# Kernel optimization log

Hardware: AMD Instinct MI355X
Metric: run time of the kernel (lower is better)

The kernel has to match this reference:

```python
import jax, jax.numpy as jnp
import numpy as np

# Custom floating-point formats (mptorch qpt.float_quantize, nearest, subnormals, no saturate)
EXP_W, MAN_W = 4, 3      # weight_quant / input_quant (e4m3)
EXP_MAC, MAN_MAC = 5, 10 # fwd MAC / bias format (e5m10, fp16-like)

B, S, D = 8, 2048, 1024
H = 4 * D


def float_quantize(x, exp, man):
    """Round x to nearest value in a float format with `exp` exponent bits and
    `man` mantissa bits, with subnormals, no saturation (overflow -> inf)."""
    bias = 2 ** (exp - 1) - 1
    min_exp = 1 - bias                      # smallest normal exponent
    max_val = (2.0 - 2.0 ** (-man)) * 2.0 ** bias
    ax = jnp.abs(x)
    e = jnp.floor(jnp.log2(jnp.where(ax > 0, ax, 1.0)))
    e = jnp.maximum(e, float(min_exp))      # clamp -> subnormal spacing
    scale = jnp.exp2(e - man)               # ulp at this exponent
    q = jnp.round(x / scale) * scale        # round-half-to-even, like 'nearest'
    q = jnp.where(jnp.abs(q) > max_val, jnp.sign(x) * jnp.inf, q)
    return jnp.where(ax == 0, x, q)


def setup_inputs() -> dict:
    key = jax.random.key(0)
    k = jax.random.split(key, 5)
    return {
        "x": jax.random.normal(k[0], (B, S, D), dtype=jnp.float32),
        "w1": jax.random.normal(k[1], (H, D), dtype=jnp.float32) * 0.02,
        "b1": jax.random.normal(k[2], (H,), dtype=jnp.float32) * 0.02,
        "w2": jax.random.normal(k[3], (D, H), dtype=jnp.float32) * 0.02,
        "b2": jax.random.normal(k[4], (D,), dtype=jnp.float32) * 0.02,
    }


def reference(x, w1, b1, w2, b2):
    # nn.Linear + ReLU (full precision)
    h = jax.nn.relu(jnp.einsum('bsd,hd->bsh', x, w1) + b1)
    # QLinear: quantize input and weight to e4m3, bias to MAC format,
    # accumulate, then quantize the result to the fwd MAC format.
    hq = float_quantize(h, EXP_W, MAN_W)
    wq = float_quantize(w2, EXP_W, MAN_W)
    bq = float_quantize(b2, EXP_MAC, MAN_MAC)
    out = jnp.einsum('bsh,dh->bsd', hq, wq) + bq
    out = float_quantize(out, EXP_MAC, MAN_MAC)
    # Dropout(0.2) is identity at inference.
    return out
```

## Files before the change

### kernel.cpp

```cpp
#include <hip/hip_runtime.h>
#include <stdint.h>


#define M_TOT 16384
#define D_DIM 1024
#define H_DIM 4096

typedef _Float16 f16x8 __attribute__((ext_vector_type(8)));
typedef _Float16 f16x4 __attribute__((ext_vector_type(4)));
typedef float f32x4 __attribute__((ext_vector_type(4)));
typedef int i32x4 __attribute__((ext_vector_type(4)));
typedef int i32x8 __attribute__((ext_vector_type(8)));

__device__ __forceinline__ void gl16(const void* g, void* l) {
    __builtin_amdgcn_global_load_lds(
        (const __attribute__((address_space(1))) unsigned int*)(uintptr_t)g,
        (__attribute__((address_space(3))) unsigned int*)(unsigned int)(uintptr_t)l,
        16, 0, 0);
}

__device__ __forceinline__ _Float16 q_e4m3_pos(float v) {
    uint32_t t = __float_as_uint(v);
    uint32_t tn = (t + 0x7ffffu + ((t >> 20) & 1u)) & 0xfff00000u;
    float qn = __uint_as_float(tn);
    float qs = rintf(v * 512.0f) * 0.001953125f;
    return (_Float16)(v < 0.015625f ? qs : qn);
}

__global__ __launch_bounds__(256) void cvt_f16_kernel(
    const float* __restrict__ in, _Float16* __restrict__ out, int n4)
{
    int i = blockIdx.x * 256 + threadIdx.x;
    if (i >= n4) return;
    float4 v = reinterpret_cast<const float4*>(in)[i];
    f16x4 hv = {(_Float16)v.x, (_Float16)v.y, (_Float16)v.z, (_Float16)v.w};
    reinterpret_cast<f16x4*>(out)[i] = hv;
}

__global__ __launch_bounds__(256) void quant_e4m3_byte_kernel(
    const float* __restrict__ in, uint32_t* __restrict__ outq, int n4)
{
    int i = blockIdx.x * 256 + threadIdx.x;
    if (i >= n4) return;
    float4 v = reinterpret_cast<const float4*>(in)[i];
    uint32_t r = __builtin_amdgcn_cvt_pk_fp8_f32(v.x, v.y, 0, false);
    r = __builtin_amdgcn_cvt_pk_fp8_f32(v.z, v.w, r, true);
    outq[i] = r;
}

__global__ __launch_bounds__(512) void gemm1_f16(
    const _Float16* __restrict__ A, const _Float16* __restrict__ B,
    const float* __restrict__ bias, uint8_t* __restrict__ Cq)
{
    constexpr int K = D_DIM;
    constexpr int N = H_DIM;
    __shared__ __align__(16) _Float16 smem[65536];
    _Float16* sA = smem;
    _Float16* sB = smem + 32768;

    const int tid  = threadIdx.x;
    const int lane = tid & 63;
    const int w    = tid >> 6;
    const int wr   = w >> 2, wc = w & 3;
    const int fr   = lane & 15, kq = lane >> 4;

    constexpr int NBX = N / 256;
    constexpr int NWG = (M_TOT / 256) * NBX;
    constexpr int CPX = NWG / 8;
    int bid = blockIdx.y * NBX + blockIdx.x;
    bid = (bid & 7) * CPX + (bid >> 3);
    const int n0 = (bid % NBX) * 256;
    const int m0 = (bid / NBX) * 256;

    const int srow = tid >> 3;
    const int sseg = (tid & 7) ^ (srow & 7);
    const _Float16* gA = A + (size_t)(m0 + srow) * K + sseg * 8;
    const _Float16* gB = B + (size_t)(n0 + srow) * K + sseg * 8;
    const int ldsw = w * 512;
    const size_t R1 = (size_t)64 * K, R2 = (size_t)128 * K, R3 = (size_t)192 * K;

    const int xorv = fr & 7;
    const int cA0 = (kq ^ xorv) * 8;
    const int cA1 = ((kq + 4) ^ xorv) * 8;
    const int aRow = wr * 128 + fr;
    const int bRow = wc * 64 + fr;

    f32x4 acc[8][4];
#pragma unroll
    for (int i = 0; i < 8; i++)
#pragma unroll
        for (int j = 0; j < 4; j++) acc[i][j] = (f32x4){0.f, 0.f, 0.f, 0.f};

    f16x8 bfr[4][2];
    constexpr int NK = K / 64;

    gl16(gB,      sB + ldsw);
    gl16(gB + R1, sB + 4096 + ldsw);
    gl16(gB + R2, sB + 8192 + ldsw);
    gl16(gB + R3, sB + 12288 + ldsw);
    gl16(gA,      sA + ldsw);
    gl16(gA + R1, sA + 4096 + ldsw);
    gl16(gA + R2, sA + 8192 + ldsw);
    gl16(gA + R3, sA + 12288 + ldsw);
    asm volatile("s_waitcnt vmcnt(0)" ::: "memory");
    __builtin_amdgcn_s_barrier();
    asm volatile("" ::: "memory");

    for (int t = 0; t < NK; ++t) {
        const int c = t & 1;
        const _Float16* sAc = sA + c * 16384;
        const _Float16* sBc = sB + c * 16384;
        _Float16* sAn = sA + (c ^ 1) * 16384;
        _Float16* sBn = sB + (c ^ 1) * 16384;
        const bool pref = (t + 1 < NK);

        if (pref) {
            const _Float16* gAn = gA + (size_t)(t + 1) * 64;
            const _Float16* gBn = gB + (size_t)(t + 1) * 64;
            gl16(gBn,      sBn + ldsw);
            gl16(gBn + R1, sBn + 4096 + ldsw);
            gl16(gBn + R2, sBn + 8192 + ldsw);
            gl16(gBn + R3, sBn + 12288 + ldsw);
            gl16(gAn,      sAn + ldsw);
            gl16(gAn + R1, sAn + 4096 + ldsw);
            gl16(gAn + R2, sAn + 8192 + ldsw);
            gl16(gAn + R3, sAn + 12288 + ldsw);
        }

#pragma unroll
        for (int p = 0; p < 4; ++p) {
            f16x8 afr[2][2];
#pragma unroll
            for (int ii = 0; ii < 2; ii++) {
                const _Float16* ra = sAc + (aRow + (2 * p + ii) * 16) * 64;
                afr[ii][0] = *(const f16x8*)(ra + cA0);
                afr[ii][1] = *(const f16x8*)(ra + cA1);
            }
            if (p == 0) {
#pragma unroll
                for (int j = 0; j < 4; j++) {
                    const _Float16* rb = sBc + (bRow + j * 16) * 64;
                    bfr[j][0] = *(const f16x8*)(rb + cA0);
                    bfr[j][1] = *(const f16x8*)(rb + cA1);
                }
            }
            __builtin_amdgcn_s_setprio(1);
#pragma unroll
            for (int ii = 0; ii < 2; ii++)
#pragma unroll
                for (int j = 0; j < 4; j++) {
                    acc[2*p+ii][j] = __builtin_amdgcn_mfma_f32_16x16x32_f16(
                        afr[ii][0], bfr[j][0], acc[2*p+ii][j], 0, 0, 0);
                    acc[2*p+ii][j] = __builtin_amdgcn_mfma_f32_16x16x32_f16(
                        afr[ii][1], bfr[j][1], acc[2*p+ii][j], 0, 0, 0);
                }
            __builtin_amdgcn_s_setprio(0);
        }

        asm volatile("s_waitcnt vmcnt(0)" ::: "memory");
        __builtin_amdgcn_s_barrier();
        asm volatile("" ::: "memory");
    }

    const int col0 = n0 + wc * 64 + fr;
    float bv[4];
#pragma unroll
    for (int j = 0; j < 4; j++) bv[j] = bias[col0 + j * 16];
    const int sub = (fr & 7) * 2;
    const int slotbase = wc * 8 + (fr >> 3);
    const int rowbase = wr * 128 + kq * 4;
#pragma unroll
    for (int i = 0; i < 8; i++) {
        const int trow0 = rowbase + i * 16;
#pragma unroll
        for (int r = 0; r < 4; r++) {
            const int trow = trow0 + r;
            const int swz = (((kq & 1) * 4 + r)) ^ (kq >> 1);
#pragma unroll
            for (int j = 0; j < 4; j++) {
                float v = fmaxf(acc[i][j][r] + bv[j], 0.0f);
                _Float16 q = q_e4m3_pos(v);
                int byte = trow * 512 + (((slotbase + j * 2) ^ swz) << 4) + sub;
                *(_Float16*)((char*)smem + byte) = q;
            }
        }
    }
    __syncthreads();
#pragma unroll
    for (int cch = 0; cch < 16; cch++) {
        int flat = cch * 512 + tid;
        int row  = flat >> 5;
        int slot = flat & 31;
        int swz  = (row & 7) ^ ((row >> 3) & 1);
        f16x8 v8 = *(const f16x8*)((char*)smem + row * 512 + ((slot ^ swz) << 4));
        uint32_t u0 = __builtin_amdgcn_cvt_pk_fp8_f32((float)v8[0], (float)v8[1], 0, false);
        u0 = __builtin_amdgcn_cvt_pk_fp8_f32((float)v8[2], (float)v8[3], u0, true);
        uint32_t u1 = __builtin_amdgcn_cvt_pk_fp8_f32((float)v8[4], (float)v8[5], 0, false);
        u1 = __builtin_amdgcn_cvt_pk_fp8_f32((float)v8[6], (float)v8[7], u1, true);
        uint2 u = {u0, u1};
        *(uint2*)(Cq + (size_t)(m0 + row) * N + n0 + slot * 8) = u;
    }
}

__global__ __launch_bounds__(512) void gemm2_fp8(
    const uint8_t* __restrict__ A, const uint8_t* __restrict__ B,
    const float* __restrict__ b2, float* __restrict__ C)
{
    constexpr int Kb = H_DIM;
    constexpr int N  = D_DIM;
    __shared__ __align__(16) uint8_t smem[131072];
    uint8_t* sA = smem;
    uint8_t* sB = smem + 65536;

    const int tid  = threadIdx.x;
    const int lane = tid & 63;
    const int w    = tid >> 6;
    const int wr   = w >> 2, wc = w & 3;
    const int fr   = lane & 15, kq = lane >> 4;

    constexpr int NBX = N / 256;
    constexpr int NWG = (M_TOT / 256) * NBX;
    constexpr int CPX = NWG / 8;
    int bid = blockIdx.y * NBX + blockIdx.x;
    bid = (bid & 7) * CPX + (bid >> 3);
    const int n0 = (bid % NBX) * 256;
    const int m0 = (bid / NBX) * 256;

    const int srow = tid >> 3;
    const int sseg = (tid & 7) ^ (srow & 7);
    const uint8_t* gA = A + (size_t)(m0 + srow) * Kb + sseg * 16;
    const uint8_t* gB = B + (size_t)(n0 + srow) * Kb + sseg * 16;
    const int ldsw = w * 1024;
    const size_t R1 = (size_t)64 * Kb, R2 = (size_t)128 * Kb, R3 = (size_t)192 * Kb;

    const int xorv = fr & 7;
    const int sO0 = ((2 * kq) ^ xorv) * 16;
    const int sO1 = ((2 * kq + 1) ^ xorv) * 16;
    const int aRowB = (wr * 128 + fr) * 128;
    const int bRowB = (wc * 64 + fr) * 128;

    f32x4 acc[8][4];
#pragma unroll
    for (int i = 0; i < 8; i++)
#pragma unroll
        for (int j = 0; j < 4; j++) acc[i][j] = (f32x4){0.f, 0.f, 0.f, 0.f};

    i32x8 bfr[4];
    constexpr int NK = Kb / 128;
    constexpr uint32_t SC1 = 0x7f7f7f7fu;

    gl16(gB,      sB + ldsw);
    gl16(gB + R1, sB + 8192 + ldsw);
    gl16(gB + R2, sB + 16384 + ldsw);
    gl16(gB + R3, sB + 24576 + ldsw);
    gl16(gA,      sA + ldsw);
    gl16(gA + R1, sA + 8192 + ldsw);
    gl16(gA + R2, sA + 16384 + ldsw);
    gl16(gA + R3, sA + 24576 + ldsw);
    asm volatile("s_waitcnt vmcnt(0)" ::: "memory");
    __builtin_amdgcn_s_barrier();
    asm volatile("" ::: "memory");

    for (int t = 0; t < NK; ++t) {
        const int c = t & 1;
        const uint8_t* sAc = sA + c * 32768;
        const uint8_t* sBc = sB + c * 32768;
        uint8_t* sAn = sA + (c ^ 1) * 32768;
        uint8_t* sBn = sB + (c ^ 1) * 32768;
        const bool pref = (t + 1 < NK);

        if (pref) {
            const uint8_t* gAn = gA + (size_t)(t + 1) * 128;
            const uint8_t* gBn = gB + (size_t)(t + 1) * 128;
            gl16(gBn,      sBn + ldsw);
            gl16(gBn + R1, sBn + 8192 + ldsw);
            gl16(gBn + R2, sBn + 16384 + ldsw);
            gl16(gBn + R3, sBn + 24576 + ldsw);
            gl16(gAn,      sAn + ldsw);
            gl16(gAn + R1, sAn + 8192 + ldsw);
            gl16(gAn + R2, sAn + 16384 + ldsw);
            gl16(gAn + R3, sAn + 24576 + ldsw);
        }

#pragma unroll
        for (int p = 0; p < 4; ++p) {
            i32x8 af[2];
#pragma unroll
            for (int ii = 0; ii < 2; ii++) {
                const uint8_t* ra = sAc + aRowB + (2 * p + ii) * 2048;
                i32x4 lo = *(const i32x4*)(ra + sO0);
                i32x4 hi = *(const i32x4*)(ra + sO1);
                af[ii] = (i32x8){lo.x, lo.y, lo.z, lo.w, hi.x, hi.y, hi.z, hi.w};
            }
            if (p == 0) {
#pragma unroll
                for (int j = 0; j < 4; j++) {
                    const uint8_t* rb = sBc + bRowB + j * 2048;
                    i32x4 lo = *(const i32x4*)(rb + sO0);
                    i32x4 hi = *(const i32x4*)(rb + sO1);
                    bfr[j] = (i32x8){lo.x, lo.y, lo.z, lo.w, hi.x, hi.y, hi.z, hi.w};
                }
            }
            __builtin_amdgcn_s_setprio(1);
#pragma unroll
            for (int ii = 0; ii < 2; ii++)
#pragma unroll
                for (int j = 0; j < 4; j++) {
                    acc[2*p+ii][j] = __builtin_amdgcn_mfma_scale_f32_16x16x128_f8f6f4(
                        af[ii], bfr[j], acc[2*p+ii][j],
                        0, 0,
                        0, SC1,
                        0, SC1);
                }
            __builtin_amdgcn_s_setprio(0);
        }

        asm volatile("s_waitcnt vmcnt(0)" ::: "memory");
        __builtin_amdgcn_s_barrier();
        asm volatile("" ::: "memory");
    }

    const int col0 = n0 + wc * 64 + fr;
    const int row0 = m0 + wr * 128 + kq * 4;
#pragma unroll
    for (int j = 0; j < 4; j++) {
        const float bq = (float)(_Float16)b2[col0 + j * 16];
#pragma unroll
        for (int i = 0; i < 8; i++) {
            size_t base = (size_t)(row0 + i * 16) * N + (col0 + j * 16);
#pragma unroll
            for (int r = 0; r < 4; r++) {
                float v = acc[i][j][r] + bq;
                C[base + (size_t)r * N] = (float)(_Float16)v;
            }
        }
    }
}

extern "C" void kernel_launch(void* const* d_in, const int* in_sizes, int n_in,
                              void* d_out, int out_size, void* d_ws, size_t ws_size,
                              hipStream_t stream) {
    const float* x  = (const float*)d_in[0];
    const float* w1 = (const float*)d_in[1];
    const float* b1 = (const float*)d_in[2];
    const float* w2 = (const float*)d_in[3];
    const float* b2 = (const float*)d_in[4];
    float* out = (float*)d_out;

    const size_t need = 67108864ull + 33554432ull + 8388608ull + 4194304ull;
    if (ws_size < need) return;

    char* ws = (char*)d_ws;
    uint8_t*  hq  = (uint8_t*)ws;
    _Float16* xh  = (_Float16*)(ws + 67108864ull);
    _Float16* w1h = xh + 16777216;
    uint8_t*  wq  = (uint8_t*)(w1h + 4194304);

    cvt_f16_kernel<<<16384, 256, 0, stream>>>(x, xh, 4194304);
    cvt_f16_kernel<<<4096, 256, 0, stream>>>(w1, w1h, 1048576);
    quant_e4m3_byte_kernel<<<4096, 256, 0, stream>>>(w2, (uint32_t*)wq, 1048576);

    gemm1_f16<<<dim3(H_DIM / 256, M_TOT / 256), 512, 0, stream>>>(xh, w1h, b1, hq);
    gemm2_fp8<<<dim3(D_DIM / 256, M_TOT / 256), 512, 0, stream>>>(hq, wq, b2, out);
}
```

Before: 246.2 us.

## Single-buffer gemm1 LDS and split epilogue staging to halve shared memory

```diff
diff --git a/kernel.cpp b/kernel.cpp
--- a/kernel.cpp
+++ b/kernel.cpp
@@ -48,15 +48,15 @@
     outq[i] = r;
 }
 
-__global__ __launch_bounds__(512) void gemm1_f16(
+__global__ __launch_bounds__(512, 4) void gemm1_f16(
     const _Float16* __restrict__ A, const _Float16* __restrict__ B,
     const float* __restrict__ bias, uint8_t* __restrict__ Cq)
 {
     constexpr int K = D_DIM;
     constexpr int N = H_DIM;
-    __shared__ __align__(16) _Float16 smem[65536];
+    __shared__ __align__(16) _Float16 smem[32768];
     _Float16* sA = smem;
-    _Float16* sB = smem + 32768;
+    _Float16* sB = smem + 16384;
 
     const int tid  = threadIdx.x;
     const int lane = tid & 63;
@@ -107,39 +107,19 @@
     asm volatile("" ::: "memory");
 
     for (int t = 0; t < NK; ++t) {
-        const int c = t & 1;
-        const _Float16* sAc = sA + c * 16384;
-        const _Float16* sBc = sB + c * 16384;
-        _Float16* sAn = sA + (c ^ 1) * 16384;
-        _Float16* sBn = sB + (c ^ 1) * 16384;
-        const bool pref = (t + 1 < NK);
-
-        if (pref) {
-            const _Float16* gAn = gA + (size_t)(t + 1) * 64;
-            const _Float16* gBn = gB + (size_t)(t + 1) * 64;
-            gl16(gBn,      sBn + ldsw);
-            gl16(gBn + R1, sBn + 4096 + ldsw);
-            gl16(gBn + R2, sBn + 8192 + ldsw);
-            gl16(gBn + R3, sBn + 12288 + ldsw);
-            gl16(gAn,      sAn + ldsw);
-            gl16(gAn + R1, sAn + 4096 + ldsw);
-            gl16(gAn + R2, sAn + 8192 + ldsw);
-            gl16(gAn + R3, sAn + 12288 + ldsw);
-        }
-
 #pragma unroll
         for (int p = 0; p < 4; ++p) {
             f16x8 afr[2][2];
 #pragma unroll
             for (int ii = 0; ii < 2; ii++) {
-                const _Float16* ra = sAc + (aRow + (2 * p + ii) * 16) * 64;
+                const _Float16* ra = sA + (aRow + (2 * p + ii) * 16) * 64;
                 afr[ii][0] = *(const f16x8*)(ra + cA0);
                 afr[ii][1] = *(const f16x8*)(ra + cA1);
             }
             if (p == 0) {
 #pragma unroll
                 for (int j = 0; j < 4; j++) {
-                    const _Float16* rb = sBc + (bRow + j * 16) * 64;
+                    const _Float16* rb = sB + (bRow + j * 16) * 64;
                     bfr[j][0] = *(const f16x8*)(rb + cA0);
                     bfr[j][1] = *(const f16x8*)(rb + cA1);
                 }
@@ -157,9 +137,25 @@
             __builtin_amdgcn_s_setprio(0);
         }
 
-        asm volatile("s_waitcnt vmcnt(0)" ::: "memory");
+        asm volatile("" ::: "memory");
         __builtin_amdgcn_s_barrier();
         asm volatile("" ::: "memory");
+
+        if (t + 1 < NK) {
+            const _Float16* gAn = gA + (size_t)(t + 1) * 64;
+            const _Float16* gBn = gB + (size_t)(t + 1) * 64;
+            gl16(gBn,      sB + ldsw);
+            gl16(gBn + R1, sB + 4096 + ldsw);
+            gl16(gBn + R2, sB + 8192 + ldsw);
+            gl16(gBn + R3, sB + 12288 + ldsw);
+            gl16(gAn,      sA + ldsw);
+            gl16(gAn + R1, sA + 4096 + ldsw);
+            gl16(gAn + R2, sA + 8192 + ldsw);
+            gl16(gAn + R3, sA + 12288 + ldsw);
+            asm volatile("s_waitcnt vmcnt(0)" ::: "memory");
+            __builtin_amdgcn_s_barrier();
+            asm volatile("" ::: "memory");
+        }
     }
 
     const int col0 = n0 + wc * 64 + fr;
@@ -168,37 +164,43 @@
     for (int j = 0; j < 4; j++) bv[j] = bias[col0 + j * 16];
     const int sub = (fr & 7) * 2;
     const int slotbase = wc * 8 + (fr >> 3);
-    const int rowbase = wr * 128 + kq * 4;
-#pragma unroll
-    for (int i = 0; i < 8; i++) {
-        const int trow0 = rowbase + i * 16;
-#pragma unroll
-        for (int r = 0; r < 4; r++) {
-            const int trow = trow0 + r;
-            const int swz = (((kq & 1) * 4 + r)) ^ (kq >> 1);
-#pragma unroll
-            for (int j = 0; j < 4; j++) {
-                float v = fmaxf(acc[i][j][r] + bv[j], 0.0f);
-                _Float16 q = q_e4m3_pos(v);
-                int byte = trow * 512 + (((slotbase + j * 2) ^ swz) << 4) + sub;
-                *(_Float16*)((char*)smem + byte) = q;
-            }
-        }
-    }
-    __syncthreads();
-#pragma unroll
-    for (int cch = 0; cch < 16; cch++) {
-        int flat = cch * 512 + tid;
-        int row  = flat >> 5;
-        int slot = flat & 31;
-        int swz  = (row & 7) ^ ((row >> 3) & 1);
-        f16x8 v8 = *(const f16x8*)((char*)smem + row * 512 + ((slot ^ swz) << 4));
-        uint32_t u0 = __builtin_amdgcn_cvt_pk_fp8_f32((float)v8[0], (float)v8[1], 0, false);
-        u0 = __builtin_amdgcn_cvt_pk_fp8_f32((float)v8[2], (float)v8[3], u0, true);
-        uint32_t u1 = __builtin_amdgcn_cvt_pk_fp8_f32((float)v8[4], (float)v8[5], 0, false);
-        u1 = __builtin_amdgcn_cvt_pk_fp8_f32((float)v8[6], (float)v8[7], u1, true);
-        uint2 u = {u0, u1};
-        *(uint2*)(Cq + (size_t)(m0 + row) * N + n0 + slot * 8) = u;
+    const int rowrel0 = kq * 4;
+#pragma unroll
+    for (int half = 0; half < 2; ++half) {
+        if (wr == half) {
+#pragma unroll
+            for (int i = 0; i < 8; i++) {
+                const int trow0 = rowrel0 + i * 16;
+#pragma unroll
+                for (int r = 0; r < 4; r++) {
+                    const int trow = trow0 + r;
+                    const int swz = ((kq & 1) * 4 + r) ^ (kq >> 1);
+#pragma unroll
+                    for (int j = 0; j < 4; j++) {
+                        float v = fmaxf(acc[i][j][r] + bv[j], 0.0f);
+                        _Float16 q = q_e4m3_pos(v);
+                        int byte = trow * 512 + (((slotbase + j * 2) ^ swz) << 4) + sub;
+                        *(_Float16*)((char*)smem + byte) = q;
+                    }
+                }
+            }
+        }
+        __syncthreads();
+#pragma unroll
+        for (int cch = 0; cch < 8; cch++) {
+            int flat = cch * 512 + tid;
+            int row  = flat >> 5;
+            int slot = flat & 31;
+            int swz  = (row & 7) ^ ((row >> 3) & 1);
+            f16x8 v8 = *(const f16x8*)((char*)smem + row * 512 + ((slot ^ swz) << 4));
+            uint32_t u0 = __builtin_amdgcn_cvt_pk_fp8_f32((float)v8[0], (float)v8[1], 0, false);
+            u0 = __builtin_amdgcn_cvt_pk_fp8_f32((float)v8[2], (float)v8[3], u0, true);
+            uint32_t u1 = __builtin_amdgcn_cvt_pk_fp8_f32((float)v8[4], (float)v8[5], 0, false);
+            u1 = __builtin_amdgcn_cvt_pk_fp8_f32((float)v8[6], (float)v8[7], u1, true);
+            uint2 u = {u0, u1};
+            *(uint2*)(Cq + (size_t)(m0 + half * 128 + row) * N + n0 + slot * 8) = u;
+        }
+        if (half == 0) __syncthreads();
     }
 }
 
```

Measured after the change: 837.6 us. 3.4x slower.

## Use 4 waves per block with 128x128 warp tiles in both GEMMs

Applied to the files above, without the earlier changes.

```diff
diff --git a/kernel.cpp b/kernel.cpp
--- a/kernel.cpp
+++ b/kernel.cpp
@@ -48,7 +48,7 @@
     outq[i] = r;
 }
 
-__global__ __launch_bounds__(512) void gemm1_f16(
+__global__ __launch_bounds__(256) void gemm1_f16(
     const _Float16* __restrict__ A, const _Float16* __restrict__ B,
     const float* __restrict__ bias, uint8_t* __restrict__ Cq)
 {
@@ -61,7 +61,7 @@
     const int tid  = threadIdx.x;
     const int lane = tid & 63;
     const int w    = tid >> 6;
-    const int wr   = w >> 2, wc = w & 3;
+    const int wr   = w >> 1, wc = w & 1;
     const int fr   = lane & 15, kq = lane >> 4;
 
     constexpr int NBX = N / 256;
@@ -77,31 +77,25 @@
     const _Float16* gA = A + (size_t)(m0 + srow) * K + sseg * 8;
     const _Float16* gB = B + (size_t)(n0 + srow) * K + sseg * 8;
     const int ldsw = w * 512;
-    const size_t R1 = (size_t)64 * K, R2 = (size_t)128 * K, R3 = (size_t)192 * K;
 
     const int xorv = fr & 7;
     const int cA0 = (kq ^ xorv) * 8;
     const int cA1 = ((kq + 4) ^ xorv) * 8;
     const int aRow = wr * 128 + fr;
-    const int bRow = wc * 64 + fr;
-
-    f32x4 acc[8][4];
+    const int bRow = wc * 128 + fr;
+
+    f32x4 acc[8][8];
 #pragma unroll
     for (int i = 0; i < 8; i++)
 #pragma unroll
-        for (int j = 0; j < 4; j++) acc[i][j] = (f32x4){0.f, 0.f, 0.f, 0.f};
-
-    f16x8 bfr[4][2];
+        for (int j = 0; j < 8; j++) acc[i][j] = (f32x4){0.f, 0.f, 0.f, 0.f};
+
     constexpr int NK = K / 64;
 
-    gl16(gB,      sB + ldsw);
-    gl16(gB + R1, sB + 4096 + ldsw);
-    gl16(gB + R2, sB + 8192 + ldsw);
-    gl16(gB + R3, sB + 12288 + ldsw);
-    gl16(gA,      sA + ldsw);
-    gl16(gA + R1, sA + 4096 + ldsw);
-    gl16(gA + R2, sA + 8192 + ldsw);
-    gl16(gA + R3, sA + 12288 + ldsw);
+#pragma unroll
+    for (int g = 0; g < 8; g++) gl16(gB + (size_t)(32 * g) * K, sB + g * 2048 + ldsw);
+#pragma unroll
+    for (int g = 0; g < 8; g++) gl16(gA + (size_t)(32 * g) * K, sA + g * 2048 + ldsw);
     asm volatile("s_waitcnt vmcnt(0)" ::: "memory");
     __builtin_amdgcn_s_barrier();
     asm volatile("" ::: "memory");
@@ -117,44 +111,32 @@
         if (pref) {
             const _Float16* gAn = gA + (size_t)(t + 1) * 64;
             const _Float16* gBn = gB + (size_t)(t + 1) * 64;
-            gl16(gBn,      sBn + ldsw);
-            gl16(gBn + R1, sBn + 4096 + ldsw);
-            gl16(gBn + R2, sBn + 8192 + ldsw);
-            gl16(gBn + R3, sBn + 12288 + ldsw);
-            gl16(gAn,      sAn + ldsw);
-            gl16(gAn + R1, sAn + 4096 + ldsw);
-            gl16(gAn + R2, sAn + 8192 + ldsw);
-            gl16(gAn + R3, sAn + 12288 + ldsw);
-        }
-
-#pragma unroll
-        for (int p = 0; p < 4; ++p) {
-            f16x8 afr[2][2];
-#pragma unroll
-            for (int ii = 0; ii < 2; ii++) {
-                const _Float16* ra = sAc + (aRow + (2 * p + ii) * 16) * 64;
-                afr[ii][0] = *(const f16x8*)(ra + cA0);
-                afr[ii][1] = *(const f16x8*)(ra + cA1);
+#pragma unroll
+            for (int g = 0; g < 8; g++) gl16(gBn + (size_t)(32 * g) * K, sBn + g * 2048 + ldsw);
+#pragma unroll
+            for (int g = 0; g < 8; g++) gl16(gAn + (size_t)(32 * g) * K, sAn + g * 2048 + ldsw);
+        }
+
+#pragma unroll
+        for (int ks = 0; ks < 2; ++ks) {
+            const int ck = ks ? cA1 : cA0;
+            f16x8 bfr[8];
+#pragma unroll
+            for (int j = 0; j < 8; j++)
+                bfr[j] = *(const f16x8*)(sBc + (bRow + j * 16) * 64 + ck);
+            f16x8 a[2];
+            a[0] = *(const f16x8*)(sAc + aRow * 64 + ck);
+#pragma unroll
+            for (int i = 0; i < 8; ++i) {
+                const int cur = i & 1, nxt = cur ^ 1;
+                if (i < 7)
+                    a[nxt] = *(const f16x8*)(sAc + (aRow + (i + 1) * 16) * 64 + ck);
+                __builtin_amdgcn_sched_barrier(0);
+#pragma unroll
+                for (int j = 0; j < 8; j++)
+                    acc[i][j] = __builtin_amdgcn_mfma_f32_16x16x32_f16(
+                        a[cur], bfr[j], acc[i][j], 0, 0, 0);
             }
-            if (p == 0) {
-#pragma unroll
-                for (int j = 0; j < 4; j++) {
-                    const _Float16* rb = sBc + (bRow + j * 16) * 64;
-                    bfr[j][0] = *(const f16x8*)(rb + cA0);
-                    bfr[j][1] = *(const f16x8*)(rb + cA1);
-                }
-            }
-            __builtin_amdgcn_s_setprio(1);
-#pragma unroll
-            for (int ii = 0; ii < 2; ii++)
-#pragma unroll
-                for (int j = 0; j < 4; j++) {
-                    acc[2*p+ii][j] = __builtin_amdgcn_mfma_f32_16x16x32_f16(
-                        afr[ii][0], bfr[j][0], acc[2*p+ii][j], 0, 0, 0);
-                    acc[2*p+ii][j] = __builtin_amdgcn_mfma_f32_16x16x32_f16(
-                        afr[ii][1], bfr[j][1], acc[2*p+ii][j], 0, 0, 0);
-                }
-            __builtin_amdgcn_s_setprio(0);
         }
 
         asm volatile("s_waitcnt vmcnt(0)" ::: "memory");
@@ -162,47 +144,53 @@
         asm volatile("" ::: "memory");
     }
 
-    const int col0 = n0 + wc * 64 + fr;
-    float bv[4];
-#pragma unroll
-    for (int j = 0; j < 4; j++) bv[j] = bias[col0 + j * 16];
+    const int col0 = n0 + wc * 128 + fr;
+    float bv[8];
+#pragma unroll
+    for (int j = 0; j < 8; j++) bv[j] = bias[col0 + j * 16];
     const int sub = (fr & 7) * 2;
-    const int slotbase = wc * 8 + (fr >> 3);
-    const int rowbase = wr * 128 + kq * 4;
-#pragma unroll
-    for (int i = 0; i < 8; i++) {
-        const int trow0 = rowbase + i * 16;
-#pragma unroll
-        for (int r = 0; r < 4; r++) {
-            const int trow = trow0 + r;
-            const int swz = (((kq & 1) * 4 + r)) ^ (kq >> 1);
-#pragma unroll
-            for (int j = 0; j < 4; j++) {
-                float v = fmaxf(acc[i][j][r] + bv[j], 0.0f);
-                _Float16 q = q_e4m3_pos(v);
-                int byte = trow * 512 + (((slotbase + j * 2) ^ swz) << 4) + sub;
-                *(_Float16*)((char*)smem + byte) = q;
+    const int slotbase = wc * 16 + (fr >> 3);
+    const int rowrel0 = kq * 4;
+#pragma unroll
+    for (int half = 0; half < 2; ++half) {
+        if (wr == half) {
+#pragma unroll
+            for (int i = 0; i < 8; i++) {
+                const int trow0 = rowrel0 + i * 16;
+#pragma unroll
+                for (int r = 0; r < 4; r++) {
+                    const int trow = trow0 + r;
+                    const int swz = ((kq & 1) * 4 + r) ^ (kq >> 1);
+#pragma unroll
+                    for (int j = 0; j < 8; j++) {
+                        float v = fmaxf(acc[i][j][r] + bv[j], 0.0f);
+                        _Float16 q = q_e4m3_pos(v);
+                        int byte = trow * 512 + (((slotbase + j * 2) ^ swz) << 4) + sub;
+                        *(_Float16*)((char*)smem + byte) = q;
+                    }
+                }
             }
         }
+        __syncthreads();
+#pragma unroll
+        for (int cch = 0; cch < 16; cch++) {
+            int flat = cch * 256 + tid;
+            int row  = flat >> 5;
+            int slot = flat & 31;
+            int swz  = (row & 7) ^ ((row >> 3) & 1);
+            f16x8 v8 = *(const f16x8*)((char*)smem + row * 512 + ((slot ^ swz) << 4));
+            uint32_t u0 = __builtin_amdgcn_cvt_pk_fp8_f32((float)v8[0], (float)v8[1], 0, false);
+            u0 = __builtin_amdgcn_cvt_pk_fp8_f32((float)v8[2], (float)v8[3], u0, true);
+            uint32_t u1 = __builtin_amdgcn_cvt_pk_fp8_f32((float)v8[4], (float)v8[5], 0, false);
+            u1 = __builtin_amdgcn_cvt_pk_fp8_f32((float)v8[6], (float)v8[7], u1, true);
+            uint2 u = {u0, u1};
+            *(uint2*)(Cq + (size_t)(m0 + half * 128 + row) * N + n0 + slot * 8) = u;
+        }
+        if (half == 0) __syncthreads();
     }
-    __syncthreads();
-#pragma unroll
-    for (int cch = 0; cch < 16; cch++) {
-        int flat = cch * 512 + tid;
-        int row  = flat >> 5;
-        int slot = flat & 31;
-        int swz  = (row & 7) ^ ((row >> 3) & 1);
-        f16x8 v8 = *(const f16x8*)((char*)smem + row * 512 + ((slot ^ swz) << 4));
-        uint32_t u0 = __builtin_amdgcn_cvt_pk_fp8_f32((float)v8[0], (float)v8[1], 0, false);
-        u0 = __builtin_amdgcn_cvt_pk_fp8_f32((float)v8[2], (float)v8[3], u0, true);
-        uint32_t u1 = __builtin_amdgcn_cvt_pk_fp8_f32((float)v8[4], (float)v8[5], 0, false);
-        u1 = __builtin_amdgcn_cvt_pk_fp8_f32((float)v8[6], (float)v8[7], u1, true);
-        uint2 u = {u0, u1};
-        *(uint2*)(Cq + (size_t)(m0 + row) * N + n0 + slot * 8) = u;
-    }
-}
-
-__global__ __launch_bounds__(512) void gemm2_fp8(
+}
+
+__global__ __launch_bounds__(256) void gemm2_fp8(
     const uint8_t* __restrict__ A, const uint8_t* __restrict__ B,
     const float* __restrict__ b2, float* __restrict__ C)
 {
@@ -215,7 +203,7 @@
     const int tid  = threadIdx.x;
     const int lane = tid & 63;
     const int w    = tid >> 6;
-    const int wr   = w >> 2, wc = w & 3;
+    const int wr   = w >> 1, wc = w & 1;
     const int fr   = lane & 15, kq = lane >> 4;
 
     constexpr int NBX = N / 256;
@@ -231,32 +219,26 @@
     const uint8_t* gA = A + (size_t)(m0 + srow) * Kb + sseg * 16;
     const uint8_t* gB = B + (size_t)(n0 + srow) * Kb + sseg * 16;
     const int ldsw = w * 1024;
-    const size_t R1 = (size_t)64 * Kb, R2 = (size_t)128 * Kb, R3 = (size_t)192 * Kb;
 
     const int xorv = fr & 7;
     const int sO0 = ((2 * kq) ^ xorv) * 16;
     const int sO1 = ((2 * kq + 1) ^ xorv) * 16;
     const int aRowB = (wr * 128 + fr) * 128;
-    const int bRowB = (wc * 64 + fr) * 128;
-
-    f32x4 acc[8][4];
+    const int bRowB = (wc * 128 + fr) * 128;
+
+    f32x4 acc[8][8];
 #pragma unroll
     for (int i = 0; i < 8; i++)
 #pragma unroll
-        for (int j = 0; j < 4; j++) acc[i][j] = (f32x4){0.f, 0.f, 0.f, 0.f};
-
-    i32x8 bfr[4];
+        for (int j = 0; j < 8; j++) acc[i][j] = (f32x4){0.f, 0.f, 0.f, 0.f};
+
     constexpr int NK = Kb / 128;
     constexpr uint32_t SC1 = 0x7f7f7f7fu;
 
-    gl16(gB,      sB + ldsw);
-    gl16(gB + R1, sB + 8192 + ldsw);
-    gl16(gB + R2, sB + 16384 + ldsw);
-    gl16(gB + R3, sB + 24576 + ldsw);
-    gl16(gA,      sA + ldsw);
-    gl16(gA + R1, sA + 8192 + ldsw);
-    gl16(gA + R2, sA + 16384 + ldsw);
-    gl16(gA + R3, sA + 24576 + ldsw);
+#pragma unroll
+    for (int g = 0; g < 8; g++) gl16(gB + (size_t)(32 * g) * Kb, sB + g * 4096 + ldsw);
+#pragma unroll
+    for (int g = 0; g < 8; g++) gl16(gA + (size_t)(32 * g) * Kb, sA + g * 4096 + ldsw);
     asm volatile("s_waitcnt vmcnt(0)" ::: "memory");
     __builtin_amdgcn_s_barrier();
     asm volatile("" ::: "memory");
@@ -272,47 +254,44 @@
         if (pref) {
             const uint8_t* gAn = gA + (size_t)(t + 1) * 128;
             const uint8_t* gBn = gB + (size_t)(t + 1) * 128;
-            gl16(gBn,      sBn + ldsw);
-            gl16(gBn + R1, sBn + 8192 + ldsw);
-            gl16(gBn + R2, sBn + 16384 + ldsw);
-            gl16(gBn + R3, sBn + 24576 + ldsw);
-            gl16(gAn,      sAn + ldsw);
-            gl16(gAn + R1, sAn + 8192 + ldsw);
-            gl16(gAn + R2, sAn + 16384 + ldsw);
-            gl16(gAn + R3, sAn + 24576 + ldsw);
-        }
-
-#pragma unroll
-        for (int p = 0; p < 4; ++p) {
-            i32x8 af[2];
-#pragma unroll
-            for (int ii = 0; ii < 2; ii++) {
-                const uint8_t* ra = sAc + aRowB + (2 * p + ii) * 2048;
+#pragma unroll
+            for (int g = 0; g < 8; g++) gl16(gBn + (size_t)(32 * g) * Kb, sBn + g * 4096 + ldsw);
+#pragma unroll
+            for (int g = 0; g < 8; g++) gl16(gAn + (size_t)(32 * g) * Kb, sAn + g * 4096 + ldsw);
+        }
+
+        i32x8 bfr[8];
+#pragma unroll
+        for (int j = 0; j < 8; j++) {
+            const uint8_t* rb = sBc + bRowB + j * 2048;
+            i32x4 lo = *(const i32x4*)(rb + sO0);
+            i32x4 hi = *(const i32x4*)(rb + sO1);
+            bfr[j] = (i32x8){lo.x, lo.y, lo.z, lo.w, hi.x, hi.y, hi.z, hi.w};
+        }
+        i32x8 a[2];
+        {
+            const uint8_t* ra = sAc + aRowB;
+            i32x4 lo = *(const i32x4*)(ra + sO0);
+            i32x4 hi = *(const i32x4*)(ra + sO1);
+            a[0] = (i32x8){lo.x, lo.y, lo.z, lo.w, hi.x, hi.y, hi.z, hi.w};
+        }
+#pragma unroll
+        for (int i = 0; i < 8; ++i) {
+            const int cur = i & 1, nxt = cur ^ 1;
+            if (i < 7) {
+                const uint8_t* ra = sAc + aRowB + (i + 1) * 2048;
                 i32x4 lo = *(const i32x4*)(ra + sO0);
                 i32x4 hi = *(const i32x4*)(ra + sO1);
-                af[ii] = (i32x8){lo.x, lo.y, lo.z, lo.w, hi.x, hi.y, hi.z, hi.w};
+                a[nxt] = (i32x8){lo.x, lo.y, lo.z, lo.w, hi.x, hi.y, hi.z, hi.w};
             }
-            if (p == 0) {
-#pragma unroll
-                for (int j = 0; j < 4; j++) {
-                    const uint8_t* rb = sBc + bRowB + j * 2048;
-                    i32x4 lo = *(const i32x4*)(rb + sO0);
-                    i32x4 hi = *(const i32x4*)(rb + sO1);
-                    bfr[j] = (i32x8){lo.x, lo.y, lo.z, lo.w, hi.x, hi.y, hi.z, hi.w};
-                }
-            }
-            __builtin_amdgcn_s_setprio(1);
-#pragma unroll
-            for (int ii = 0; ii < 2; ii++)
-#pragma unroll
-                for (int j = 0; j < 4; j++) {
-                    acc[2*p+ii][j] = __builtin_amdgcn_mfma_scale_f32_16x16x128_f8f6f4(
-                        af[ii], bfr[j], acc[2*p+ii][j],
-                        0, 0,
-                        0, SC1,
-                        0, SC1);
-                }
-            __builtin_amdgcn_s_setprio(0);
+            __builtin_amdgcn_sched_barrier(0);
+#pragma unroll
+            for (int j = 0; j < 8; j++)
+                acc[i][j] = __builtin_amdgcn_mfma_scale_f32_16x16x128_f8f6f4(
+                    a[cur], bfr[j], acc[i][j],
+                    0, 0,
+                    0, SC1,
+                    0, SC1);
         }
 
         asm volatile("s_waitcnt vmcnt(0)" ::: "memory");
@@ -320,10 +299,10 @@
         asm volatile("" ::: "memory");
     }
 
-    const int col0 = n0 + wc * 64 + fr;
+    const int col0 = n0 + wc * 128 + fr;
     const int row0 = m0 + wr * 128 + kq * 4;
 #pragma unroll
-    for (int j = 0; j < 4; j++) {
+    for (int j = 0; j < 8; j++) {
         const float bq = (float)(_Float16)b2[col0 + j * 16];
 #pragma unroll
         for (int i = 0; i < 8; i++) {
@@ -360,6 +339,6 @@
     cvt_f16_kernel<<<4096, 256, 0, stream>>>(w1, w1h, 1048576);
     quant_e4m3_byte_kernel<<<4096, 256, 0, stream>>>(w2, (uint32_t*)wq, 1048576);
 
-    gemm1_f16<<<dim3(H_DIM / 256, M_TOT / 256), 512, 0, stream>>>(xh, w1h, b1, hq);
-    gemm2_fp8<<<dim3(D_DIM / 256, M_TOT / 256), 512, 0, stream>>>(hq, wq, b2, out);
-}
+    gemm1_f16<<<dim3(H_DIM / 256, M_TOT / 256), 256, 0, stream>>>(xh, w1h, b1, hq);
+    gemm2_fp8<<<dim3(D_DIM / 256, M_TOT / 256), 256, 0, stream>>>(hq, wq, b2, out);
+}
```

Result: slower. 284.7 us (+15.6%).
